# Kernel tuning notes

Hardware: AMD Instinct MI355X
Metric: run time of the kernel (lower is better)

The kernel has to match this reference:

```python
import jax, jax.numpy as jnp
import numpy as np

N_NODES = 100000
N_EDGES = 1280000
D_IN = 64
D_OUT = 64


def setup_inputs() -> dict:
    key = jax.random.key(0)
    k_x, k_e, k_w, k_rw = jax.random.split(key, 4)
    x = jax.random.normal(k_x, (N_NODES, D_IN), dtype=jnp.float32)
    edge_index = jax.random.randint(k_e, (2, N_EDGES), 0, N_NODES, dtype=jnp.int32)
    glorot = float(np.sqrt(6.0 / (D_IN + D_OUT)))
    weight = jax.random.uniform(k_w, (D_IN, D_OUT), dtype=jnp.float32, minval=-glorot, maxval=glorot)
    root_weight = jax.random.uniform(k_rw, (D_IN, D_OUT), dtype=jnp.float32, minval=-glorot, maxval=glorot)
    bias = jnp.zeros((D_OUT,), dtype=jnp.float32)
    return {"x": x, "edge_index": edge_index, "weight": weight,
            "root_weight": root_weight, "bias": bias}


def reference(x, edge_index, weight, root_weight, bias):
    # adj_0 = SparseTensor(row=edge_index[0], col=edge_index[1])
    # adj_0.matmul(x, reduce='mean'): out[i] = mean_{(i,j) in E} x[j]
    n = x.shape[0]
    row, col = edge_index[0], edge_index[1]
    msg = x[col]                                              # [E, D_in] gather
    summed = jax.ops.segment_sum(msg, row, num_segments=n)    # [N, D_in]
    count = jax.ops.segment_sum(jnp.ones((row.shape[0],), dtype=x.dtype), row,
                                num_segments=n)               # [N]
    agg = summed / jnp.maximum(count, 1.0)[:, None]           # mean (deg-0 -> 0)
    out = agg @ weight + x @ root_weight + bias
    return out
```

## Files before the change

kernel.cpp:

```cpp
#include <hip/hip_runtime.h>
#include <hip/hip_bf16.h>

#define N_NODES 100000
#define N_EDGES 1280000
#define D 64
#define NB ((N_NODES + 255) / 256)
#define NBKT 391
#define BKT_SHIFT 8
#define BKT_NODES 256
#define CAP 3712
#define COL_PAD 4096
#define BIN_EPB 4096
#define BIN_BLOCKS 313
#define PRE_BLOCKS 782

using short8 = __attribute__((ext_vector_type(8))) short;
using f32x4  = __attribute__((ext_vector_type(4))) float;

__device__ __forceinline__ unsigned short f2bf(float f) {
    unsigned int u = __float_as_uint(f);
    unsigned int r = (u + 0x7FFFu + ((u >> 16) & 1u)) >> 16;
    return (unsigned short)r;
}

__device__ __forceinline__ float bf2f(unsigned short u) {
    union { unsigned int i; float f; } v;
    v.i = ((unsigned int)u) << 16;
    return v.f;
}

__global__ void zero_bcnt_kernel(int* __restrict__ bcnt) {
    int t = threadIdx.x;
    if (t < NBKT) bcnt[t] = 0;
}

__launch_bounds__(512)
__global__ void bin_pre_kernel(const int* __restrict__ row,
                               const int* __restrict__ col,
                               int* __restrict__ bucket_cnt,
                               unsigned int* __restrict__ pairs,
                               const float* __restrict__ x,
                               const float* __restrict__ W,
                               const float* __restrict__ Wr,
                               const float* __restrict__ bias,
                               unsigned int* __restrict__ y_packed,
                               float* __restrict__ out) {
    __shared__ __align__(16) char smem[22784];
    int tid = threadIdx.x;

    if (blockIdx.x < BIN_BLOCKS) {
        unsigned int* sorted = (unsigned int*)smem;
        int* cnt   = (int*)(smem + 16384);
        int* lexcl = cnt + NBKT;
        int* lcur  = lexcl + NBKT;
        int* gbase = lcur + NBKT;
        int* wsum  = gbase + NBKT;
        int* wexcl = wsum + 8;

        for (int i = tid; i < NBKT; i += 512) cnt[i] = 0;
        __syncthreads();

        int rr[8], cc[8];
#pragma unroll
        for (int i = 0; i < 8; ++i) {
            int e = blockIdx.x * BIN_EPB + i * 512 + tid;
            if (e < N_EDGES) {
                rr[i] = row[e];
                cc[i] = col[e];
                atomicAdd(&cnt[rr[i] >> BKT_SHIFT], 1);
            } else {
                rr[i] = -1;
            }
        }
        __syncthreads();

        int lane = tid & 63, wv = tid >> 6;
        int v = (tid < NBKT) ? cnt[tid] : 0;
        int incl = v;
#pragma unroll
        for (int d = 1; d < 64; d <<= 1) {
            int u = __shfl_up(incl, d, 64);
            if (lane >= d) incl += u;
        }
        if (lane == 63) wsum[wv] = incl;
        __syncthreads();
        if (tid < 8) {
            int w = wsum[tid];
            int p = w;
#pragma unroll
            for (int d = 1; d < 8; d <<= 1) {
                int u = __shfl_up(p, d, 64);
                if (tid >= d) p += u;
            }
            wexcl[tid] = p - w;
        }
        __syncthreads();
        if (tid < NBKT) {
            int excl = incl - v + wexcl[wv];
            lexcl[tid] = excl;
            lcur[tid]  = excl;
            if (v > 0) gbase[tid] = atomicAdd(&bucket_cnt[tid], v);
        }
        __syncthreads();

#pragma unroll
        for (int i = 0; i < 8; ++i) {
            if (rr[i] >= 0) {
                int b = rr[i] >> BKT_SHIFT;
                int slot = atomicAdd(&lcur[b], 1);
                sorted[slot] = ((unsigned int)(rr[i] & (BKT_NODES - 1)) << 17)
                             | (unsigned int)cc[i];
            }
        }
        __syncthreads();

        int grp = tid >> 4, l16 = tid & 15;
        for (int bb = grp; bb < NBKT; bb += 32) {
            int len = cnt[bb];
            if (len == 0) continue;
            int src = lexcl[bb];
            int dst = gbase[bb];
            for (int k = l16; k < len; k += 16) {
                int gs = dst + k;
                if (gs < CAP)
                    pairs[(size_t)bb * CAP + gs] = sorted[src + k];
            }
        }
    } else {
        unsigned short* Wl = (unsigned short*)smem;

        for (int idx = tid; idx < 8192; idx += 512) {
            int j    = idx & 7;
            int lane = (idx >> 3) & 63;
            int h    = (idx >> 9) & 1;
            int t    = (idx >> 10) & 3;
            int mat  = idx >> 12;
            int k = h * 32 + ((lane >> 4) << 3) + j;
            int n = t * 16 + (lane & 15);
            const float* src = mat ? Wr : W;
            Wl[idx] = f2bf(src[k * D + n]);
        }
        __syncthreads();

        int wv = tid >> 6;
        int lane = tid & 63;
        int g = (blockIdx.x - BIN_BLOCKS) * 8 + wv;
        if (g >= N_NODES / 16) return;

        int quad = lane >> 4;
        int n16 = lane & 15;
        int m_node = g * 16 + n16;

        short8 A[2];
#pragma unroll
        for (int h = 0; h < 2; ++h) {
            const float* xr = x + (size_t)m_node * D + h * 32 + quad * 8;
            float4 xa = *(const float4*)xr;
            float4 xb = *(const float4*)(xr + 4);
            short8 a;
            a[0] = (short)f2bf(xa.x); a[1] = (short)f2bf(xa.y);
            a[2] = (short)f2bf(xa.z); a[3] = (short)f2bf(xa.w);
            a[4] = (short)f2bf(xb.x); a[5] = (short)f2bf(xb.y);
            a[6] = (short)f2bf(xb.z); a[7] = (short)f2bf(xb.w);
            A[h] = a;
        }

        int row0 = g * 16 + quad * 4;

#pragma unroll
        for (int t = 0; t < 4; ++t) {
            short8 By0 = *(const short8*)&Wl[(((0 * 4 + t) * 2 + 0) * 64 + lane) * 8];
            short8 By1 = *(const short8*)&Wl[(((0 * 4 + t) * 2 + 1) * 64 + lane) * 8];
            short8 Bz0 = *(const short8*)&Wl[(((1 * 4 + t) * 2 + 0) * 64 + lane) * 8];
            short8 Bz1 = *(const short8*)&Wl[(((1 * 4 + t) * 2 + 1) * 64 + lane) * 8];

            f32x4 accY = {0.f, 0.f, 0.f, 0.f};
            accY = __builtin_amdgcn_mfma_f32_16x16x32_bf16(A[0], By0, accY, 0, 0, 0);
            accY = __builtin_amdgcn_mfma_f32_16x16x32_bf16(A[1], By1, accY, 0, 0, 0);
            f32x4 accZ = {0.f, 0.f, 0.f, 0.f};
            accZ = __builtin_amdgcn_mfma_f32_16x16x32_bf16(A[0], Bz0, accZ, 0, 0, 0);
            accZ = __builtin_amdgcn_mfma_f32_16x16x32_bf16(A[1], Bz1, accZ, 0, 0, 0);

            float bv = bias[t * 16 + n16];
#pragma unroll
            for (int r = 0; r < 4; ++r) {
                out[(size_t)(row0 + r) * D + t * 16 + n16] = accZ[r] + bv;
                unsigned int me = f2bf(accY[r]);
                unsigned int nb = (unsigned int)__shfl_xor((int)me, 1, 64) & 0xFFFFu;
                if ((lane & 1) == 0)
                    y_packed[((size_t)(row0 + r) * D + t * 16 + n16) >> 1] = me | (nb << 16);
            }
        }
    }
}

__launch_bounds__(1024, 8)
__global__ void csr_gather_kernel(const unsigned short* __restrict__ yu,
                                  const unsigned int* __restrict__ pairs,
                                  const int* __restrict__ bucket_cnt,
                                  float* __restrict__ out) {
    __shared__ int col_lds[COL_PAD];
    __shared__ int deg_s[BKT_NODES];
    __shared__ int start_s[BKT_NODES];
    __shared__ int lcur[BKT_NODES];
    __shared__ int cnt_s[BKT_NODES];
    __shared__ int wsum[4];

    int b = blockIdx.x;
    int tid = threadIdx.x;
    int m = bucket_cnt[b];
    if (m > CAP) m = CAP;
    const unsigned int* pb = pairs + (size_t)b * CAP;

    if (tid < BKT_NODES) cnt_s[tid] = 0;
    __syncthreads();

    uint4 p4 = ((const uint4*)pb)[tid];
    bool v0 = (4 * tid + 0) < m, v1 = (4 * tid + 1) < m,
         v2 = (4 * tid + 2) < m, v3 = (4 * tid + 3) < m;
    if (v0) atomicAdd(&cnt_s[p4.x >> 17], 1);
    if (v1) atomicAdd(&cnt_s[p4.y >> 17], 1);
    if (v2) atomicAdd(&cnt_s[p4.z >> 17], 1);
    if (v3) atomicAdd(&cnt_s[p4.w >> 17], 1);
    __syncthreads();

    if (tid < BKT_NODES) {
        int v = cnt_s[tid];
        int incl = v;
        for (int d = 1; d < 64; d <<= 1) {
            int t = __shfl_up(incl, d, 64);
            if ((tid & 63) >= d) incl += t;
        }
        if ((tid & 63) == 63) wsum[tid >> 6] = incl;
        deg_s[tid] = v;
        cnt_s[tid] = incl;
    }
    __syncthreads();
    if (tid < BKT_NODES) {
        int w = tid >> 6;
        int pre = 0;
        if (w > 0) pre += wsum[0];
        if (w > 1) pre += wsum[1];
        if (w > 2) pre += wsum[2];
        int excl = cnt_s[tid] + pre - deg_s[tid];
        start_s[tid] = excl;
        lcur[tid] = excl;
    }
    __syncthreads();

    if (v0) { int r = (int)(p4.x >> 17); int c = (int)(p4.x & 0x1FFFFu);
              col_lds[atomicAdd(&lcur[r], 1)] = c < N_NODES ? c : 0; }
    if (v1) { int r = (int)(p4.y >> 17); int c = (int)(p4.y & 0x1FFFFu);
              col_lds[atomicAdd(&lcur[r], 1)] = c < N_NODES ? c : 0; }
    if (v2) { int r = (int)(p4.z >> 17); int c = (int)(p4.z & 0x1FFFFu);
              col_lds[atomicAdd(&lcur[r], 1)] = c < N_NODES ? c : 0; }
    if (v3) { int r = (int)(p4.w >> 17); int c = (int)(p4.w & 0x1FFFFu);
              col_lds[atomicAdd(&lcur[r], 1)] = c < N_NODES ? c : 0; }
    __syncthreads();

    int wv = tid >> 6;
    int lane = tid & 63;
    int s = lane >> 4;
    int q = lane & 15;

#pragma unroll 1
    for (int pk = 0; pk < 4; ++pk) {
        int n0 = wv * 16 + pk * 4;
        int nvx = deg_s[n0 + 0], nvy = deg_s[n0 + 1],
            nvz = deg_s[n0 + 2], nvw = deg_s[n0 + 3];
        int st0 = start_s[n0 + 0], st1 = start_s[n0 + 1],
            st2 = start_s[n0 + 2], st3 = start_s[n0 + 3];

        float4 a0 = make_float4(0.f, 0.f, 0.f, 0.f);
        float4 a1 = a0, a2 = a0, a3 = a0;

        {
            int mm = nvx > nvy ? nvx : nvy;
            for (int j = 0; j < mm; j += 4) {
                int jj = j + s;
                int c0 = col_lds[(st0 + jj) & (COL_PAD - 1)];
                int c1 = col_lds[(st1 + jj) & (COL_PAD - 1)];
                c0 = (jj < nvx) ? c0 : 0;
                c1 = (jj < nvy) ? c1 : 0;
                ushort4 u0 = *(const ushort4*)&yu[(size_t)c0 * D + q * 4];
                ushort4 u1 = *(const ushort4*)&yu[(size_t)c1 * D + q * 4];
                if (jj < nvx) {
                    a0.x += bf2f(u0.x); a0.y += bf2f(u0.y);
                    a0.z += bf2f(u0.z); a0.w += bf2f(u0.w);
                }
                if (jj < nvy) {
                    a1.x += bf2f(u1.x); a1.y += bf2f(u1.y);
                    a1.z += bf2f(u1.z); a1.w += bf2f(u1.w);
                }
            }
        }
        {
            int mm = nvz > nvw ? nvz : nvw;
            for (int j = 0; j < mm; j += 4) {
                int jj = j + s;
                int c2 = col_lds[(st2 + jj) & (COL_PAD - 1)];
                int c3 = col_lds[(st3 + jj) & (COL_PAD - 1)];
                c2 = (jj < nvz) ? c2 : 0;
                c3 = (jj < nvw) ? c3 : 0;
                ushort4 u2 = *(const ushort4*)&yu[(size_t)c2 * D + q * 4];
                ushort4 u3 = *(const ushort4*)&yu[(size_t)c3 * D + q * 4];
                if (jj < nvz) {
                    a2.x += bf2f(u2.x); a2.y += bf2f(u2.y);
                    a2.z += bf2f(u2.z); a2.w += bf2f(u2.w);
                }
                if (jj < nvw) {
                    a3.x += bf2f(u3.x); a3.y += bf2f(u3.y);
                    a3.z += bf2f(u3.z); a3.w += bf2f(u3.w);
                }
            }
        }

#define BFLY(a) \
    a.x += __shfl_xor(a.x, 16, 64); a.y += __shfl_xor(a.y, 16, 64); \
    a.z += __shfl_xor(a.z, 16, 64); a.w += __shfl_xor(a.w, 16, 64); \
    a.x += __shfl_xor(a.x, 32, 64); a.y += __shfl_xor(a.y, 32, 64); \
    a.z += __shfl_xor(a.z, 32, 64); a.w += __shfl_xor(a.w, 32, 64);
        BFLY(a0) BFLY(a1) BFLY(a2) BFLY(a3)
#undef BFLY

        float inv0 = 1.0f / (float)(nvx > 1 ? nvx : 1);
        float inv1 = 1.0f / (float)(nvy > 1 ? nvy : 1);
        float inv2 = 1.0f / (float)(nvz > 1 ? nvz : 1);
        float inv3 = 1.0f / (float)(nvw > 1 ? nvw : 1);

        float4 rr = (s == 0) ? a0 : (s == 1) ? a1 : (s == 2) ? a2 : a3;
        float invs = (s == 0) ? inv0 : (s == 1) ? inv1 : (s == 2) ? inv2 : inv3;
        int g = (b << BKT_SHIFT) + n0 + s;
        if (g < N_NODES) {
            size_t off = (size_t)g * D + q * 4;
            float4 z = *(const float4*)&out[off];
            z.x += rr.x * invs; z.y += rr.y * invs;
            z.z += rr.z * invs; z.w += rr.w * invs;
            *(float4*)&out[off] = z;
        }
    }
}


__global__ void hist_kernel(const int4* __restrict__ row4, int* __restrict__ deg) {
    int t = blockIdx.x * blockDim.x + threadIdx.x;
    if (t < N_EDGES / 4) {
        int4 r = row4[t];
        atomicAdd(&deg[r.x], 1);
        atomicAdd(&deg[r.y], 1);
        atomicAdd(&deg[r.z], 1);
        atomicAdd(&deg[r.w], 1);
    }
}

__global__ void scan_block_kernel(const int* __restrict__ deg,
                                  int* __restrict__ cursor,
                                  int* __restrict__ bsum) {
    __shared__ int s[256];
    int tid = threadIdx.x;
    int gid = blockIdx.x * 256 + tid;
    int v = (gid < N_NODES) ? deg[gid] : 0;
    s[tid] = v;
    __syncthreads();
    for (int d = 1; d < 256; d <<= 1) {
        int t = (tid >= d) ? s[tid - d] : 0;
        __syncthreads();
        s[tid] += t;
        __syncthreads();
    }
    if (gid < N_NODES) cursor[gid] = s[tid] - v;
    if (tid == 255) bsum[blockIdx.x] = s[255];
}

__global__ void add_offsets_kernel(int* __restrict__ cursor,
                                   const int* __restrict__ bsum_raw) {
    __shared__ int red[256];
    int tid = threadIdx.x;
    int b = blockIdx.x;
    int sum = 0;
    for (int i = tid; i < b; i += 256) sum += bsum_raw[i];
    red[tid] = sum;
    __syncthreads();
    for (int off = 128; off > 0; off >>= 1) {
        if (tid < off) red[tid] += red[tid + off];
        __syncthreads();
    }
    int gid = b * 256 + tid;
    if (gid < N_NODES) cursor[gid] += red[0];
}

__global__ void scatter_build_kernel(const int4* __restrict__ row4,
                                     const int4* __restrict__ col4,
                                     int* __restrict__ cursor,
                                     int* __restrict__ col_sorted) {
    int t = blockIdx.x * blockDim.x + threadIdx.x;
    if (t < N_EDGES / 4) {
        int4 r = row4[t];
        int4 c = col4[t];
        col_sorted[atomicAdd(&cursor[r.x], 1)] = c.x;
        col_sorted[atomicAdd(&cursor[r.y], 1)] = c.y;
        col_sorted[atomicAdd(&cursor[r.z], 1)] = c.z;
        col_sorted[atomicAdd(&cursor[r.w], 1)] = c.w;
    }
}

__launch_bounds__(512, 8)
__global__ void aggregate_kernel(const float* __restrict__ x,
                                 const int* __restrict__ cursor_end,
                                 const int* __restrict__ deg,
                                 const int* __restrict__ col_sorted,
                                 const float* __restrict__ W,
                                 const float* __restrict__ Wr,
                                 const float* __restrict__ bias,
                                 float* __restrict__ out) {
    __shared__ float Ws[D * D];
    __shared__ float Wrs[D * D];
    __shared__ float agg_s[8][D];
    __shared__ float x_s[8][D];

    for (int i = threadIdx.x; i < D * D / 4; i += 512) {
        ((float4*)Ws)[i]  = ((const float4*)W)[i];
        ((float4*)Wrs)[i] = ((const float4*)Wr)[i];
    }
    __syncthreads();

    int wv = threadIdx.x >> 6;
    int lane = threadIdx.x & 63;
    int s = lane >> 4;
    int q = lane & 15;
    float bf = bias[lane];

    int node0 = (blockIdx.x * 8 + wv) * 4;

#pragma unroll 1
    for (int nn = 0; nn < 4; ++nn) {
        int r = node0 + nn;
        int n = deg[r];
        int start = cursor_end[r] - n;

        float4 acc = make_float4(0.f, 0.f, 0.f, 0.f);
        for (int base = 0; base < n; base += 64) {
            int m = n - base; if (m > 64) m = 64;
            int idx = 0;
            if (lane < m) idx = col_sorted[start + base + lane];
            for (int j = 0; j < m; j += 4) {
                int jj = j + s;
                int c = __shfl(idx, jj, 64);
                if (jj < m) {
                    float4 v = *(const float4*)&x[(size_t)c * D + q * 4];
                    acc.x += v.x; acc.y += v.y; acc.z += v.z; acc.w += v.w;
                }
            }
        }
        acc.x += __shfl_xor(acc.x, 16, 64);
        acc.y += __shfl_xor(acc.y, 16, 64);
        acc.z += __shfl_xor(acc.z, 16, 64);
        acc.w += __shfl_xor(acc.w, 16, 64);
        acc.x += __shfl_xor(acc.x, 32, 64);
        acc.y += __shfl_xor(acc.y, 32, 64);
        acc.z += __shfl_xor(acc.z, 32, 64);
        acc.w += __shfl_xor(acc.w, 32, 64);

        float inv = 1.0f / (float)(n > 1 ? n : 1);
        if (lane < 16) {
            float4 a = make_float4(acc.x * inv, acc.y * inv, acc.z * inv, acc.w * inv);
            *(float4*)&agg_s[wv][q * 4] = a;
            *(float4*)&x_s[wv][q * 4] = *(const float4*)&x[(size_t)r * D + q * 4];
        }
        __builtin_amdgcn_wave_barrier();

        int f = lane;
        float o = bf;
        const float4* av = (const float4*)agg_s[wv];
        const float4* xv = (const float4*)x_s[wv];
#pragma unroll
        for (int k4 = 0; k4 < 16; ++k4) {
            float4 a = av[k4];
            float4 xx = xv[k4];
            int k = k4 * 4;
            o += a.x * Ws[(k + 0) * D + f] + xx.x * Wrs[(k + 0) * D + f];
            o += a.y * Ws[(k + 1) * D + f] + xx.y * Wrs[(k + 1) * D + f];
            o += a.z * Ws[(k + 2) * D + f] + xx.z * Wrs[(k + 2) * D + f];
            o += a.w * Ws[(k + 3) * D + f] + xx.w * Wrs[(k + 3) * D + f];
        }
        out[(size_t)r * D + f] = o;
        __builtin_amdgcn_wave_barrier();
    }
}


__global__ void zero_kernel(float* __restrict__ summed, float* __restrict__ cnt) {
    int stride = gridDim.x * blockDim.x;
    int i = blockIdx.x * blockDim.x + threadIdx.x;
    const int total = N_NODES * D;
    for (int idx = i; idx < total; idx += stride) summed[idx] = 0.0f;
    for (int idx = i; idx < N_NODES; idx += stride) cnt[idx] = 0.0f;
}

__global__ void scatter_atomic_kernel(const float* __restrict__ x,
                                      const int* __restrict__ row,
                                      const int* __restrict__ col,
                                      float* __restrict__ summed,
                                      float* __restrict__ cnt) {
    long long gid = (long long)blockIdx.x * blockDim.x + threadIdx.x;
    const long long total = (long long)N_EDGES * D;
    if (gid >= total) return;
    int e = (int)(gid >> 6);
    int f = (int)(gid & 63);
    int r = row[e];
    int c = col[e];
    atomicAdd(&summed[r * D + f], x[c * D + f]);
    if (f == 0) atomicAdd(&cnt[r], 1.0f);
}

__global__ void finish_kernel(const float* __restrict__ x,
                              const float* __restrict__ W,
                              const float* __restrict__ Wr,
                              const float* __restrict__ bias,
                              const float* __restrict__ cnt,
                              float* __restrict__ out) {
    __shared__ float agg_s[4][D];
    __shared__ float x_s[4][D];
    int lrow = threadIdx.x >> 6;
    int f = threadIdx.x & 63;
    int r = blockIdx.x * 4 + lrow;

    float c = cnt[r];
    float inv = 1.0f / fmaxf(c, 1.0f);
    agg_s[lrow][f] = out[r * D + f] * inv;
    x_s[lrow][f] = x[r * D + f];
    __syncthreads();

    float acc = bias[f];
#pragma unroll 8
    for (int k = 0; k < D; ++k) {
        acc += agg_s[lrow][k] * W[k * D + f];
        acc += x_s[lrow][k] * Wr[k * D + f];
    }
    out[r * D + f] = acc;
}


extern "C" void kernel_launch(void* const* d_in, const int* in_sizes, int n_in,
                              void* d_out, int out_size, void* d_ws, size_t ws_size,
                              hipStream_t stream) {
    const float* x    = (const float*)d_in[0];
    const int*   ei   = (const int*)d_in[1];
    const float* W    = (const float*)d_in[2];
    const float* Wr   = (const float*)d_in[3];
    const float* bias = (const float*)d_in[4];
    float* out = (float*)d_out;

    const int* row = ei;
    const int* col = ei + N_EDGES;

    const size_t t1_cnt   = 0;
    const size_t t1_pairs = 2048;
    const size_t t1_y     = 2048 + (size_t)NBKT * CAP * 4;
    const size_t t1_need  = t1_y + (size_t)N_NODES * D * 2;

    const size_t csr_bytes = (size_t)2 * N_NODES * 4 + 2048 + (size_t)N_EDGES * 4;

    if (ws_size >= t1_need) {
        char* ws = (char*)d_ws;
        int* bcnt = (int*)(ws + t1_cnt);
        unsigned int* pairs    = (unsigned int*)(ws + t1_pairs);
        unsigned int* y_packed = (unsigned int*)(ws + t1_y);

        zero_bcnt_kernel<<<1, 512, 0, stream>>>(bcnt);
        bin_pre_kernel<<<BIN_BLOCKS + PRE_BLOCKS, 512, 0, stream>>>(
            row, col, bcnt, pairs, x, W, Wr, bias, y_packed, out);
        csr_gather_kernel<<<NBKT, 1024, 0, stream>>>(
            (const unsigned short*)y_packed, pairs, bcnt, out);
    } else if (ws_size >= csr_bytes) {
        char* ws = (char*)d_ws;
        int* deg        = (int*)(ws);
        int* cursor     = (int*)(ws + (size_t)1 * N_NODES * 4);
        int* bsum       = (int*)(ws + (size_t)2 * N_NODES * 4);
        int* col_sorted = (int*)(ws + (size_t)2 * N_NODES * 4 + 2048);

        hipMemsetAsync(deg, 0, (size_t)N_NODES * 4, stream);
        hist_kernel<<<(N_EDGES / 4 + 255) / 256, 256, 0, stream>>>((const int4*)row, deg);
        scan_block_kernel<<<NB, 256, 0, stream>>>(deg, cursor, bsum);
        add_offsets_kernel<<<NB, 256, 0, stream>>>(cursor, bsum);
        scatter_build_kernel<<<(N_EDGES / 4 + 255) / 256, 256, 0, stream>>>(
            (const int4*)row, (const int4*)col, cursor, col_sorted);
        aggregate_kernel<<<N_NODES / 32, 512, 0, stream>>>(x, cursor, deg, col_sorted, W, Wr, bias, out);
    } else {
        float* cnt = (float*)d_ws;
        zero_kernel<<<4096, 256, 0, stream>>>(out, cnt);
        long long total = (long long)N_EDGES * D;
        int blocks = (int)((total + 255) / 256);
        scatter_atomic_kernel<<<blocks, 256, 0, stream>>>(x, row, col, out, cnt);
        finish_kernel<<<(N_NODES + 3) / 4, 256, 0, stream>>>(x, W, Wr, bias, cnt, out);
    }
}
```

Before: 140.5 us.

## Fuse binning, precompute and gather into one cooperative persistent kernel

Replaces the three-launch pipeline (zero counters, bin+precompute, CSR gather) with a single cooperative kernel of 512 blocks that uses grid-wide syncs between phases. Precompute work is handed out dynamically through an atomic cursor, and the gather phase now runs 512 threads per bucket instead of 1024. The aim is to remove kernel launch gaps and tail effects. In exchange it adds grid.sync overhead, lowers parallelism in the gather phase, and falls back to the old path if the cooperative launch fails.

```diff
diff --git a/kernel.cpp b/kernel.cpp
--- a/kernel.cpp
+++ b/kernel.cpp
@@ -1,5 +1,8 @@
 #include <hip/hip_runtime.h>
 #include <hip/hip_bf16.h>
+#include <hip/hip_cooperative_groups.h>
+
+namespace cg = cooperative_groups;
 
 #define N_NODES 100000
 #define N_EDGES 1280000
@@ -13,6 +16,10 @@
 #define BIN_EPB 4096
 #define BIN_BLOCKS 313
 #define PRE_BLOCKS 782
+#define CB 512
+#define CB_BIN 320
+#define EPB3 4000
+#define PRE_SETS 782
 
 using short8 = __attribute__((ext_vector_type(8))) short;
 using f32x4  = __attribute__((ext_vector_type(4))) float;
@@ -28,6 +35,343 @@
     v.i = ((unsigned int)u) << 16;
     return v.f;
 }
+
+__launch_bounds__(512, 4)
+__global__ void fused_kernel(const int* __restrict__ row,
+                             const int* __restrict__ col,
+                             int* bcnt,
+                             unsigned int* pairs,
+                             const float* __restrict__ x,
+                             const float* __restrict__ W,
+                             const float* __restrict__ Wr,
+                             const float* __restrict__ bias,
+                             unsigned int* y_packed,
+                             float* out,
+                             int* pre_cursor) {
+    cg::grid_group grid = cg::this_grid();
+    __shared__ __align__(16) char smem[22784];
+    __shared__ int bcast;
+    int tid = threadIdx.x;
+    int blk = blockIdx.x;
+    int gtid = blk * 512 + tid;
+
+    if (gtid < NBKT) atomicExch(&bcnt[gtid], 0);
+    if (gtid == NBKT) atomicExch(pre_cursor, 0);
+    grid.sync();
+
+    if (blk < CB_BIN) {
+        unsigned int* sorted = (unsigned int*)smem;
+        int* cnt   = (int*)(smem + 16000);
+        int* lexcl = cnt + NBKT;
+        int* lcur  = lexcl + NBKT;
+        int* gbase = lcur + NBKT;
+        int* wsum  = gbase + NBKT;
+        int* wexcl = wsum + 8;
+
+        for (int i = tid; i < NBKT; i += 512) cnt[i] = 0;
+        __syncthreads();
+
+        int rr[8], cc[8];
+#pragma unroll
+        for (int i = 0; i < 8; ++i) {
+            int idx = i * 512 + tid;
+            int e = blk * EPB3 + idx;
+            if (idx < EPB3) {
+                rr[i] = row[e];
+                cc[i] = col[e];
+                atomicAdd(&cnt[rr[i] >> BKT_SHIFT], 1);
+            } else {
+                rr[i] = -1;
+            }
+        }
+        __syncthreads();
+
+        int lane = tid & 63, wv = tid >> 6;
+        int v = (tid < NBKT) ? cnt[tid] : 0;
+        int incl = v;
+#pragma unroll
+        for (int d = 1; d < 64; d <<= 1) {
+            int u = __shfl_up(incl, d, 64);
+            if (lane >= d) incl += u;
+        }
+        if (lane == 63) wsum[wv] = incl;
+        __syncthreads();
+        if (tid < 8) {
+            int w = wsum[tid];
+            int p = w;
+#pragma unroll
+            for (int d = 1; d < 8; d <<= 1) {
+                int u = __shfl_up(p, d, 64);
+                if (tid >= d) p += u;
+            }
+            wexcl[tid] = p - w;
+        }
+        __syncthreads();
+        if (tid < NBKT) {
+            int excl = incl - v + wexcl[wv];
+            lexcl[tid] = excl;
+            lcur[tid]  = excl;
+            if (v > 0) gbase[tid] = atomicAdd(&bcnt[tid], v);
+        }
+        __syncthreads();
+
+#pragma unroll
+        for (int i = 0; i < 8; ++i) {
+            if (rr[i] >= 0) {
+                int b = rr[i] >> BKT_SHIFT;
+                int slot = atomicAdd(&lcur[b], 1);
+                sorted[slot] = ((unsigned int)(rr[i] & (BKT_NODES - 1)) << 17)
+                             | (unsigned int)cc[i];
+            }
+        }
+        __syncthreads();
+
+        int grp = tid >> 4, l16 = tid & 15;
+        for (int bb = grp; bb < NBKT; bb += 32) {
+            int len = cnt[bb];
+            if (len == 0) continue;
+            int src = lexcl[bb];
+            int dst = gbase[bb];
+            for (int k = l16; k < len; k += 16) {
+                int gs = dst + k;
+                if (gs < CAP)
+                    pairs[(size_t)bb * CAP + gs] = sorted[src + k];
+            }
+        }
+        __syncthreads();
+    }
+
+    {
+        unsigned short* Wl = (unsigned short*)smem;
+        for (int idx = tid; idx < 8192; idx += 512) {
+            int j    = idx & 7;
+            int lane = (idx >> 3) & 63;
+            int h    = (idx >> 9) & 1;
+            int t    = (idx >> 10) & 3;
+            int mat  = idx >> 12;
+            int k = h * 32 + ((lane >> 4) << 3) + j;
+            int n = t * 16 + (lane & 15);
+            const float* src = mat ? Wr : W;
+            Wl[idx] = f2bf(src[k * D + n]);
+        }
+        __syncthreads();
+
+        int wv = tid >> 6;
+        int lane = tid & 63;
+        int quad = lane >> 4;
+        int n16 = lane & 15;
+
+        for (;;) {
+            if (tid == 0) bcast = atomicAdd(pre_cursor, 1);
+            __syncthreads();
+            int gs = bcast;
+            if (gs >= PRE_SETS) break;
+
+            int g = gs * 8 + wv;
+            if (g < N_NODES / 16) {
+                int m_node = g * 16 + n16;
+                short8 A[2];
+#pragma unroll
+                for (int h = 0; h < 2; ++h) {
+                    const float* xr = x + (size_t)m_node * D + h * 32 + quad * 8;
+                    float4 xa = *(const float4*)xr;
+                    float4 xb = *(const float4*)(xr + 4);
+                    short8 a;
+                    a[0] = (short)f2bf(xa.x); a[1] = (short)f2bf(xa.y);
+                    a[2] = (short)f2bf(xa.z); a[3] = (short)f2bf(xa.w);
+                    a[4] = (short)f2bf(xb.x); a[5] = (short)f2bf(xb.y);
+                    a[6] = (short)f2bf(xb.z); a[7] = (short)f2bf(xb.w);
+                    A[h] = a;
+                }
+                int row0 = g * 16 + quad * 4;
+#pragma unroll
+                for (int t = 0; t < 4; ++t) {
+                    short8 By0 = *(const short8*)&Wl[(((0 * 4 + t) * 2 + 0) * 64 + lane) * 8];
+                    short8 By1 = *(const short8*)&Wl[(((0 * 4 + t) * 2 + 1) * 64 + lane) * 8];
+                    short8 Bz0 = *(const short8*)&Wl[(((1 * 4 + t) * 2 + 0) * 64 + lane) * 8];
+                    short8 Bz1 = *(const short8*)&Wl[(((1 * 4 + t) * 2 + 1) * 64 + lane) * 8];
+
+                    f32x4 accY = {0.f, 0.f, 0.f, 0.f};
+                    accY = __builtin_amdgcn_mfma_f32_16x16x32_bf16(A[0], By0, accY, 0, 0, 0);
+                    accY = __builtin_amdgcn_mfma_f32_16x16x32_bf16(A[1], By1, accY, 0, 0, 0);
+                    f32x4 accZ = {0.f, 0.f, 0.f, 0.f};
+                    accZ = __builtin_amdgcn_mfma_f32_16x16x32_bf16(A[0], Bz0, accZ, 0, 0, 0);
+                    accZ = __builtin_amdgcn_mfma_f32_16x16x32_bf16(A[1], Bz1, accZ, 0, 0, 0);
+
+                    float bv = bias[t * 16 + n16];
+#pragma unroll
+                    for (int r = 0; r < 4; ++r) {
+                        out[(size_t)(row0 + r) * D + t * 16 + n16] = accZ[r] + bv;
+                        unsigned int me = f2bf(accY[r]);
+                        unsigned int nb = (unsigned int)__shfl_xor((int)me, 1, 64) & 0xFFFFu;
+                        if ((lane & 1) == 0)
+                            y_packed[((size_t)(row0 + r) * D + t * 16 + n16) >> 1] = me | (nb << 16);
+                    }
+                }
+            }
+            __syncthreads();
+        }
+    }
+    __threadfence();
+    grid.sync();
+
+    if (blk < NBKT) {
+        int* col_lds = (int*)smem;
+        int* deg_s   = (int*)(smem + 16384);
+        int* start_s = deg_s + BKT_NODES;
+        int* lcur2   = start_s + BKT_NODES;
+        int* cnt_s   = lcur2 + BKT_NODES;
+        int* wsum2   = cnt_s + BKT_NODES;
+
+        int m = bcnt[blk];
+        if (m > CAP) m = CAP;
+        const uint4* pb4 = (const uint4*)(pairs + (size_t)blk * CAP);
+
+        if (tid < BKT_NODES) cnt_s[tid] = 0;
+        __syncthreads();
+
+        uint4 pa = pb4[tid];
+        uint4 pc = (tid < CAP / 4 - 512) ? pb4[tid + 512] : make_uint4(0u, 0u, 0u, 0u);
+        int ea = 4 * tid, ec = 2048 + 4 * tid;
+        bool a0 = ea + 0 < m, a1 = ea + 1 < m, a2 = ea + 2 < m, a3 = ea + 3 < m;
+        bool c0 = ec + 0 < m, c1 = ec + 1 < m, c2 = ec + 2 < m, c3 = ec + 3 < m;
+        if (a0) atomicAdd(&cnt_s[pa.x >> 17], 1);
+        if (a1) atomicAdd(&cnt_s[pa.y >> 17], 1);
+        if (a2) atomicAdd(&cnt_s[pa.z >> 17], 1);
+        if (a3) atomicAdd(&cnt_s[pa.w >> 17], 1);
+        if (c0) atomicAdd(&cnt_s[pc.x >> 17], 1);
+        if (c1) atomicAdd(&cnt_s[pc.y >> 17], 1);
+        if (c2) atomicAdd(&cnt_s[pc.z >> 17], 1);
+        if (c3) atomicAdd(&cnt_s[pc.w >> 17], 1);
+        __syncthreads();
+
+        if (tid < BKT_NODES) {
+            int v = cnt_s[tid];
+            int incl = v;
+            for (int d = 1; d < 64; d <<= 1) {
+                int t = __shfl_up(incl, d, 64);
+                if ((tid & 63) >= d) incl += t;
+            }
+            if ((tid & 63) == 63) wsum2[tid >> 6] = incl;
+            deg_s[tid] = v;
+            cnt_s[tid] = incl;
+        }
+        __syncthreads();
+        if (tid < BKT_NODES) {
+            int w = tid >> 6;
+            int pre = 0;
+            if (w > 0) pre += wsum2[0];
+            if (w > 1) pre += wsum2[1];
+            if (w > 2) pre += wsum2[2];
+            int excl = cnt_s[tid] + pre - deg_s[tid];
+            start_s[tid] = excl;
+            lcur2[tid] = excl;
+        }
+        __syncthreads();
+
+        if (a0) { int r = (int)(pa.x >> 17); int c = (int)(pa.x & 0x1FFFFu);
+                  col_lds[atomicAdd(&lcur2[r], 1)] = c < N_NODES ? c : 0; }
+        if (a1) { int r = (int)(pa.y >> 17); int c = (int)(pa.y & 0x1FFFFu);
+                  col_lds[atomicAdd(&lcur2[r], 1)] = c < N_NODES ? c : 0; }
+        if (a2) { int r = (int)(pa.z >> 17); int c = (int)(pa.z & 0x1FFFFu);
+                  col_lds[atomicAdd(&lcur2[r], 1)] = c < N_NODES ? c : 0; }
+        if (a3) { int r = (int)(pa.w >> 17); int c = (int)(pa.w & 0x1FFFFu);
+                  col_lds[atomicAdd(&lcur2[r], 1)] = c < N_NODES ? c : 0; }
+        if (c0) { int r = (int)(pc.x >> 17); int c = (int)(pc.x & 0x1FFFFu);
+                  col_lds[atomicAdd(&lcur2[r], 1)] = c < N_NODES ? c : 0; }
+        if (c1) { int r = (int)(pc.y >> 17); int c = (int)(pc.y & 0x1FFFFu);
+                  col_lds[atomicAdd(&lcur2[r], 1)] = c < N_NODES ? c : 0; }
+        if (c2) { int r = (int)(pc.z >> 17); int c = (int)(pc.z & 0x1FFFFu);
+                  col_lds[atomicAdd(&lcur2[r], 1)] = c < N_NODES ? c : 0; }
+        if (c3) { int r = (int)(pc.w >> 17); int c = (int)(pc.w & 0x1FFFFu);
+                  col_lds[atomicAdd(&lcur2[r], 1)] = c < N_NODES ? c : 0; }
+        __syncthreads();
+
+        int wv = tid >> 6;
+        int lane = tid & 63;
+        int s = lane >> 4;
+        int q = lane & 15;
+
+#pragma unroll 1
+        for (int pk = 0; pk < 8; ++pk) {
+            int n0 = wv * 32 + pk * 4;
+            int nvx = deg_s[n0 + 0], nvy = deg_s[n0 + 1],
+                nvz = deg_s[n0 + 2], nvw = deg_s[n0 + 3];
+            int st0 = start_s[n0 + 0], st1 = start_s[n0 + 1],
+                st2 = start_s[n0 + 2], st3 = start_s[n0 + 3];
+
+            float4 A0 = make_float4(0.f, 0.f, 0.f, 0.f);
+            float4 A1 = A0, A2 = A0, A3 = A0;
+
+            const unsigned short* yu = (const unsigned short*)y_packed;
+            {
+                int mm = nvx > nvy ? nvx : nvy;
+                for (int j = 0; j < mm; j += 4) {
+                    int jj = j + s;
+                    int cx = col_lds[(st0 + jj) & (COL_PAD - 1)];
+                    int cy = col_lds[(st1 + jj) & (COL_PAD - 1)];
+                    cx = (jj < nvx) ? cx : 0;
+                    cy = (jj < nvy) ? cy : 0;
+                    ushort4 u0 = *(const ushort4*)&yu[(size_t)cx * D + q * 4];
+                    ushort4 u1 = *(const ushort4*)&yu[(size_t)cy * D + q * 4];
+                    if (jj < nvx) {
+                        A0.x += bf2f(u0.x); A0.y += bf2f(u0.y);
+                        A0.z += bf2f(u0.z); A0.w += bf2f(u0.w);
+                    }
+                    if (jj < nvy) {
+                        A1.x += bf2f(u1.x); A1.y += bf2f(u1.y);
+                        A1.z += bf2f(u1.z); A1.w += bf2f(u1.w);
+                    }
+                }
+            }
+            {
+                int mm = nvz > nvw ? nvz : nvw;
+                for (int j = 0; j < mm; j += 4) {
+                    int jj = j + s;
+                    int cz = col_lds[(st2 + jj) & (COL_PAD - 1)];
+                    int cw = col_lds[(st3 + jj) & (COL_PAD - 1)];
+                    cz = (jj < nvz) ? cz : 0;
+                    cw = (jj < nvw) ? cw : 0;
+                    ushort4 u2 = *(const ushort4*)&yu[(size_t)cz * D + q * 4];
+                    ushort4 u3 = *(const ushort4*)&yu[(size_t)cw * D + q * 4];
+                    if (jj < nvz) {
+                        A2.x += bf2f(u2.x); A2.y += bf2f(u2.y);
+                        A2.z += bf2f(u2.z); A2.w += bf2f(u2.w);
+                    }
+                    if (jj < nvw) {
+                        A3.x += bf2f(u3.x); A3.y += bf2f(u3.y);
+                        A3.z += bf2f(u3.z); A3.w += bf2f(u3.w);
+                    }
+                }
+            }
+
+#define BFLY(a) \
+    a.x += __shfl_xor(a.x, 16, 64); a.y += __shfl_xor(a.y, 16, 64); \
+    a.z += __shfl_xor(a.z, 16, 64); a.w += __shfl_xor(a.w, 16, 64); \
+    a.x += __shfl_xor(a.x, 32, 64); a.y += __shfl_xor(a.y, 32, 64); \
+    a.z += __shfl_xor(a.z, 32, 64); a.w += __shfl_xor(a.w, 32, 64);
+            BFLY(A0) BFLY(A1) BFLY(A2) BFLY(A3)
+#undef BFLY
+
+            float inv0 = 1.0f / (float)(nvx > 1 ? nvx : 1);
+            float inv1 = 1.0f / (float)(nvy > 1 ? nvy : 1);
+            float inv2 = 1.0f / (float)(nvz > 1 ? nvz : 1);
+            float inv3 = 1.0f / (float)(nvw > 1 ? nvw : 1);
+
+            float4 rr4 = (s == 0) ? A0 : (s == 1) ? A1 : (s == 2) ? A2 : A3;
+            float invs = (s == 0) ? inv0 : (s == 1) ? inv1 : (s == 2) ? inv2 : inv3;
+            int g = (blk << BKT_SHIFT) + n0 + s;
+            if (g < N_NODES) {
+                size_t off = (size_t)g * D + q * 4;
+                float4 z = *(const float4*)&out[off];
+                z.x += rr4.x * invs; z.y += rr4.y * invs;
+                z.z += rr4.z * invs; z.w += rr4.w * invs;
+                *(float4*)&out[off] = z;
+            }
+        }
+    }
+}
+
 
 __global__ void zero_bcnt_kernel(int* __restrict__ bcnt) {
     int t = threadIdx.x;
@@ -564,14 +908,23 @@
     if (ws_size >= t1_need) {
         char* ws = (char*)d_ws;
         int* bcnt = (int*)(ws + t1_cnt);
+        int* pre_cursor = bcnt + 400;
         unsigned int* pairs    = (unsigned int*)(ws + t1_pairs);
         unsigned int* y_packed = (unsigned int*)(ws + t1_y);
 
-        zero_bcnt_kernel<<<1, 512, 0, stream>>>(bcnt);
-        bin_pre_kernel<<<BIN_BLOCKS + PRE_BLOCKS, 512, 0, stream>>>(
-            row, col, bcnt, pairs, x, W, Wr, bias, y_packed, out);
-        csr_gather_kernel<<<NBKT, 1024, 0, stream>>>(
-            (const unsigned short*)y_packed, pairs, bcnt, out);
+        void* args[] = { (void*)&row, (void*)&col, (void*)&bcnt, (void*)&pairs,
+                         (void*)&x, (void*)&W, (void*)&Wr, (void*)&bias,
+                         (void*)&y_packed, (void*)&out, (void*)&pre_cursor };
+        hipError_t err = hipLaunchCooperativeKernel(
+            fused_kernel, dim3(CB), dim3(512), args, 0, stream);
+        if (err != hipSuccess) {
+            (void)hipGetLastError();
+            zero_bcnt_kernel<<<1, 512, 0, stream>>>(bcnt);
+            bin_pre_kernel<<<BIN_BLOCKS + PRE_BLOCKS, 512, 0, stream>>>(
+                row, col, bcnt, pairs, x, W, Wr, bias, y_packed, out);
+            csr_gather_kernel<<<NBKT, 1024, 0, stream>>>(
+                (const unsigned short*)y_packed, pairs, bcnt, out);
+        }
     } else if (ws_size >= csr_bytes) {
         char* ws = (char*)d_ws;
         int* deg        = (int*)(ws);
```

Result: slower. 374.5 us (+166.5%).

## Replace global bucket atomics with per-segment offset table and coalesced segment writes

Applied to the files above, without the earlier changes.

The binning blocks no longer reserve space in per-bucket global arrays through atomics. Each block now writes its locally sorted 4096-edge segment back contiguously with uint4 stores and records each bucket's offset in a table. The gather kernel reads its bucket's slice from all 313 segments using those offsets, which removes the zeroing kernel launch, the global atomics and the fixed CAP truncation. In exchange each gather block makes many short, scattered reads across segments, and the col_lds index is masked, which could silently wrap if a bucket exceeds 4096 edges.

```diff
diff --git a/kernel.cpp b/kernel.cpp
--- a/kernel.cpp
+++ b/kernel.cpp
@@ -8,10 +8,9 @@
 #define NBKT 391
 #define BKT_SHIFT 8
 #define BKT_NODES 256
-#define CAP 3712
 #define COL_PAD 4096
-#define BIN_EPB 4096
-#define BIN_BLOCKS 313
+#define SEG_E 4096
+#define NSEG 313
 #define PRE_BLOCKS 782
 
 using short8 = __attribute__((ext_vector_type(8))) short;
@@ -29,15 +28,11 @@
     return v.f;
 }
 
-__global__ void zero_bcnt_kernel(int* __restrict__ bcnt) {
-    int t = threadIdx.x;
-    if (t < NBKT) bcnt[t] = 0;
-}
 
 __launch_bounds__(512)
 __global__ void bin_pre_kernel(const int* __restrict__ row,
                                const int* __restrict__ col,
-                               int* __restrict__ bucket_cnt,
+                               int* __restrict__ off_tab,
                                unsigned int* __restrict__ pairs,
                                const float* __restrict__ x,
                                const float* __restrict__ W,
@@ -47,24 +42,28 @@
                                float* __restrict__ out) {
     __shared__ __align__(16) char smem[22784];
     int tid = threadIdx.x;
-
-    if (blockIdx.x < BIN_BLOCKS) {
+    int blk = blockIdx.x;
+
+    if (blk < NSEG) {
         unsigned int* sorted = (unsigned int*)smem;
         int* cnt   = (int*)(smem + 16384);
         int* lexcl = cnt + NBKT;
         int* lcur  = lexcl + NBKT;
-        int* gbase = lcur + NBKT;
-        int* wsum  = gbase + NBKT;
+        int* wsum  = lcur + NBKT;
         int* wexcl = wsum + 8;
 
+        int blk_edges = N_EDGES - blk * SEG_E;
+        if (blk_edges > SEG_E) blk_edges = SEG_E;
+
         for (int i = tid; i < NBKT; i += 512) cnt[i] = 0;
         __syncthreads();
 
         int rr[8], cc[8];
 #pragma unroll
         for (int i = 0; i < 8; ++i) {
-            int e = blockIdx.x * BIN_EPB + i * 512 + tid;
-            if (e < N_EDGES) {
+            int idx = i * 512 + tid;
+            if (idx < blk_edges) {
+                int e = blk * SEG_E + idx;
                 rr[i] = row[e];
                 cc[i] = col[e];
                 atomicAdd(&cnt[rr[i] >> BKT_SHIFT], 1);
@@ -99,8 +98,9 @@
             int excl = incl - v + wexcl[wv];
             lexcl[tid] = excl;
             lcur[tid]  = excl;
-            if (v > 0) gbase[tid] = atomicAdd(&bucket_cnt[tid], v);
-        }
+            off_tab[tid * NSEG + blk] = excl;
+        }
+        if (tid == NBKT) off_tab[NBKT * NSEG + blk] = blk_edges;
         __syncthreads();
 
 #pragma unroll
@@ -114,18 +114,11 @@
         }
         __syncthreads();
 
-        int grp = tid >> 4, l16 = tid & 15;
-        for (int bb = grp; bb < NBKT; bb += 32) {
-            int len = cnt[bb];
-            if (len == 0) continue;
-            int src = lexcl[bb];
-            int dst = gbase[bb];
-            for (int k = l16; k < len; k += 16) {
-                int gs = dst + k;
-                if (gs < CAP)
-                    pairs[(size_t)bb * CAP + gs] = sorted[src + k];
-            }
-        }
+        uint4* dst = (uint4*)(pairs + (size_t)blk * SEG_E);
+        const uint4* src = (const uint4*)sorted;
+#pragma unroll
+        for (int i = 0; i < 2; ++i)
+            dst[i * 512 + tid] = src[i * 512 + tid];
     } else {
         unsigned short* Wl = (unsigned short*)smem;
 
@@ -144,7 +137,7 @@
 
         int wv = tid >> 6;
         int lane = tid & 63;
-        int g = (blockIdx.x - BIN_BLOCKS) * 8 + wv;
+        int g = (blk - NSEG) * 8 + wv;
         if (g >= N_NODES / 16) return;
 
         int quad = lane >> 4;
@@ -197,7 +190,7 @@
 __launch_bounds__(1024, 8)
 __global__ void csr_gather_kernel(const unsigned short* __restrict__ yu,
                                   const unsigned int* __restrict__ pairs,
-                                  const int* __restrict__ bucket_cnt,
+                                  const int* __restrict__ off_tab,
                                   float* __restrict__ out) {
     __shared__ int col_lds[COL_PAD];
     __shared__ int deg_s[BKT_NODES];
@@ -205,23 +198,28 @@
     __shared__ int lcur[BKT_NODES];
     __shared__ int cnt_s[BKT_NODES];
     __shared__ int wsum[4];
+    __shared__ int soff[NSEG];
+    __shared__ int slen[NSEG];
 
     int b = blockIdx.x;
     int tid = threadIdx.x;
-    int m = bucket_cnt[b];
-    if (m > CAP) m = CAP;
-    const unsigned int* pb = pairs + (size_t)b * CAP;
-
+
+    if (tid < NSEG) {
+        int s0 = off_tab[b * NSEG + tid];
+        soff[tid] = s0;
+        slen[tid] = off_tab[(b + 1) * NSEG + tid] - s0;
+    }
     if (tid < BKT_NODES) cnt_s[tid] = 0;
     __syncthreads();
 
-    uint4 p4 = ((const uint4*)pb)[tid];
-    bool v0 = (4 * tid + 0) < m, v1 = (4 * tid + 1) < m,
-         v2 = (4 * tid + 2) < m, v3 = (4 * tid + 3) < m;
-    if (v0) atomicAdd(&cnt_s[p4.x >> 17], 1);
-    if (v1) atomicAdd(&cnt_s[p4.y >> 17], 1);
-    if (v2) atomicAdd(&cnt_s[p4.z >> 17], 1);
-    if (v3) atomicAdd(&cnt_s[p4.w >> 17], 1);
+    int grp = tid >> 4, l16 = tid & 15;
+
+    for (int seg = grp; seg < NSEG; seg += 64) {
+        const unsigned int* p = pairs + (size_t)seg * SEG_E + soff[seg];
+        int len = slen[seg];
+        for (int k = l16; k < len; k += 16)
+            atomicAdd(&cnt_s[p[k] >> 17], 1);
+    }
     __syncthreads();
 
     if (tid < BKT_NODES) {
@@ -248,14 +246,16 @@
     }
     __syncthreads();
 
-    if (v0) { int r = (int)(p4.x >> 17); int c = (int)(p4.x & 0x1FFFFu);
-              col_lds[atomicAdd(&lcur[r], 1)] = c < N_NODES ? c : 0; }
-    if (v1) { int r = (int)(p4.y >> 17); int c = (int)(p4.y & 0x1FFFFu);
-              col_lds[atomicAdd(&lcur[r], 1)] = c < N_NODES ? c : 0; }
-    if (v2) { int r = (int)(p4.z >> 17); int c = (int)(p4.z & 0x1FFFFu);
-              col_lds[atomicAdd(&lcur[r], 1)] = c < N_NODES ? c : 0; }
-    if (v3) { int r = (int)(p4.w >> 17); int c = (int)(p4.w & 0x1FFFFu);
-              col_lds[atomicAdd(&lcur[r], 1)] = c < N_NODES ? c : 0; }
+    for (int seg = grp; seg < NSEG; seg += 64) {
+        const unsigned int* p = pairs + (size_t)seg * SEG_E + soff[seg];
+        int len = slen[seg];
+        for (int k = l16; k < len; k += 16) {
+            unsigned int e = p[k];
+            int r = (int)(e >> 17);
+            int c = (int)(e & 0x1FFFFu);
+            col_lds[atomicAdd(&lcur[r], 1) & (COL_PAD - 1)] = c < N_NODES ? c : 0;
+        }
+    }
     __syncthreads();
 
     int wv = tid >> 6;
@@ -554,24 +554,23 @@
     const int* row = ei;
     const int* col = ei + N_EDGES;
 
-    const size_t t1_cnt   = 0;
-    const size_t t1_pairs = 2048;
-    const size_t t1_y     = 2048 + (size_t)NBKT * CAP * 4;
+    const size_t t1_off   = 0;
+    const size_t t1_pairs = (size_t)(NBKT + 1) * NSEG * 4;
+    const size_t t1_y     = t1_pairs + (size_t)NSEG * SEG_E * 4;
     const size_t t1_need  = t1_y + (size_t)N_NODES * D * 2;
 
     const size_t csr_bytes = (size_t)2 * N_NODES * 4 + 2048 + (size_t)N_EDGES * 4;
 
     if (ws_size >= t1_need) {
         char* ws = (char*)d_ws;
-        int* bcnt = (int*)(ws + t1_cnt);
+        int* off_tab = (int*)(ws + t1_off);
         unsigned int* pairs    = (unsigned int*)(ws + t1_pairs);
         unsigned int* y_packed = (unsigned int*)(ws + t1_y);
 
-        zero_bcnt_kernel<<<1, 512, 0, stream>>>(bcnt);
-        bin_pre_kernel<<<BIN_BLOCKS + PRE_BLOCKS, 512, 0, stream>>>(
-            row, col, bcnt, pairs, x, W, Wr, bias, y_packed, out);
+        bin_pre_kernel<<<NSEG + PRE_BLOCKS, 512, 0, stream>>>(
+            row, col, off_tab, pairs, x, W, Wr, bias, y_packed, out);
         csr_gather_kernel<<<NBKT, 1024, 0, stream>>>(
-            (const unsigned short*)y_packed, pairs, bcnt, out);
+            (const unsigned short*)y_packed, pairs, off_tab, out);
     } else if (ws_size >= csr_bytes) {
         char* ws = (char*)d_ws;
         int* deg        = (int*)(ws);
```

Result: slower. 148.5 us (+5.7%).
